# Optimization experiments

Measured on AMD Instinct MI355X. Metric: run time of the kernel, lower is better.

## Reference

```python
import jax, jax.numpy as jnp
import numpy as np

B, IN, H = 65536, 256, 512

def setup_inputs() -> dict:
    key = jax.random.key(0)
    ks = jax.random.split(key, 10)
    inp = {
        "x": jax.random.normal(ks[0], (B, IN), dtype=jnp.float32),
        "h_prev": jax.random.normal(ks[1], (B, H), dtype=jnp.float32),
        "c_prev": jax.random.normal(ks[2], (B, H), dtype=jnp.float32),
        "n_prev": jax.random.uniform(ks[3], (B, H), dtype=jnp.float32),
        "m_prev": jax.random.normal(ks[4], (B, H), dtype=jnp.float32),
        "w_f": jax.random.normal(ks[5], (IN, H), dtype=jnp.float32) * 0.05,
        "w_c": jax.random.normal(ks[6], (IN, H), dtype=jnp.float32) * 0.05,
        "r_f": jax.random.normal(ks[7], (H, H), dtype=jnp.float32) * 0.05,
        "r_c": jax.random.normal(ks[8], (H, H), dtype=jnp.float32) * 0.05,
        "b_f": jnp.zeros((H,), dtype=jnp.float32),
        "b_c": jnp.zeros((H,), dtype=jnp.float32),
    }
    return inp

def reference(x, h_prev, c_prev, n_prev, m_prev, w_f, w_c, r_f, r_c, b_f, b_c):
    # f_t = exp(pre_f); log(f_t) = pre_f, so stabilizer works on pre-activations.
    pre_f = x @ w_f + h_prev @ r_f + b_f          # [B, H]
    c_tilda = x @ w_c + h_prev @ r_c + b_c        # [B, H]
    # m_t = max(log f_t + m_prev, log(exp(0))) = max(pre_f + m_prev, 0)
    m_t = jnp.maximum(pre_f + m_prev, 0.0)
    i_prime = jnp.exp(-m_t)
    f_prime = jnp.exp(pre_f + m_prev - m_t)
    c_t = f_prime * c_prev + i_prime * jnp.tanh(c_tilda)
    n_t = f_prime * n_prev + i_prime
    h_t = jnp.tanh(c_t / jnp.maximum(n_t, 1e-8))
    return (h_t, c_t, n_t, m_t)
```

## Files before the change

kernel.cpp:

```cpp
#include <hip/hip_runtime.h>

#define B_SZ   65536
#define IN_SZ  256
#define H_SZ   512
#define K_SZ   768
#define BM     128
#define BN     128
#define BK     64
#define LDK    72

typedef __attribute__((ext_vector_type(4))) float  f32x4;
typedef __attribute__((ext_vector_type(8))) __bf16 bf16x8;

__device__ __forceinline__ unsigned short f2bf(float f) {
    unsigned u = __float_as_uint(f);
    u += 0x7FFFu + ((u >> 16) & 1u);
    return (unsigned short)(u >> 16);
}

__device__ __forceinline__ float tanh_fast(float x) {
    x = fminf(fmaxf(x, -16.0f), 16.0f);
    float e = __expf(2.0f * x);
    return (e - 1.0f) / (e + 1.0f);
}

__global__ void prep_weights(const float* __restrict__ w_f, const float* __restrict__ w_c,
                             const float* __restrict__ r_f, const float* __restrict__ r_c,
                             unsigned short* __restrict__ wt) {
    int id = blockIdx.x * 256 + threadIdx.x;
    int n  = id / K_SZ;
    int k  = id - n * K_SZ;
    int col = n & (H_SZ - 1);
    float v;
    if (n < H_SZ) v = (k < IN_SZ) ? w_f[k * H_SZ + col] : r_f[(k - IN_SZ) * H_SZ + col];
    else          v = (k < IN_SZ) ? w_c[k * H_SZ + col] : r_c[(k - IN_SZ) * H_SZ + col];
    wt[(size_t)n * K_SZ + k] = f2bf(v);
}

__launch_bounds__(256, 2)
__global__ void smgu_kernel(const float* __restrict__ x, const float* __restrict__ h_prev,
                            const float* __restrict__ c_prev, const float* __restrict__ n_prev,
                            const float* __restrict__ m_prev,
                            const float* __restrict__ b_f, const float* __restrict__ b_c,
                            const unsigned short* __restrict__ wt,
                            float* __restrict__ out) {
    __shared__ unsigned short sA[BM * LDK];
    __shared__ unsigned short sF[BN * LDK];
    __shared__ unsigned short sC[BN * LDK];

    const int tid    = threadIdx.x;
    const int bid    = blockIdx.x;
    const int tile_m = bid >> 2;
    const int tile_n = bid & 3;
    const int m0 = tile_m * BM;
    const int n0 = tile_n * BN;

    const int lane = tid & 63;
    const int wave = tid >> 6;
    const int wm = (wave >> 1) * 64;
    const int wn = (wave & 1) * 64;

    const int fr = lane & 15;
    const int fg = (lane >> 4) * 8;

    f32x4 accF[4][4];
    f32x4 accC[4][4];
#pragma unroll
    for (int i = 0; i < 4; ++i)
#pragma unroll
        for (int j = 0; j < 4; ++j) { accF[i][j] = (f32x4)0.0f; accC[i][j] = (f32x4)0.0f; }

    for (int kb = 0; kb < K_SZ; kb += BK) {
        {
            const float* src; int ldsrc, kloc;
            if (kb < IN_SZ) { src = x;      ldsrc = IN_SZ; kloc = kb; }
            else            { src = h_prev; ldsrc = H_SZ;  kloc = kb - IN_SZ; }
#pragma unroll
            for (int j = 0; j < 8; ++j) {
                int idx = tid + 256 * j;
                int row = idx >> 4, c4 = idx & 15;
                const float4 v = *(const float4*)&src[(size_t)(m0 + row) * ldsrc + kloc + c4 * 4];
                ushort4 b;
                b.x = f2bf(v.x); b.y = f2bf(v.y); b.z = f2bf(v.z); b.w = f2bf(v.w);
                *(ushort4*)&sA[row * LDK + c4 * 4] = b;
            }
        }
#pragma unroll
        for (int j = 0; j < 4; ++j) {
            int idx = tid + 256 * j;
            int row = idx >> 3, c8 = idx & 7;
            uint4 vf = *(const uint4*)&wt[(size_t)(n0 + row) * K_SZ + kb + c8 * 8];
            *(uint4*)&sF[row * LDK + c8 * 8] = vf;
            uint4 vc = *(const uint4*)&wt[(size_t)(H_SZ + n0 + row) * K_SZ + kb + c8 * 8];
            *(uint4*)&sC[row * LDK + c8 * 8] = vc;
        }
        __syncthreads();

#pragma unroll
        for (int ks = 0; ks < BK; ks += 32) {
            bf16x8 af[4], bf[4], bc[4];
#pragma unroll
            for (int mi = 0; mi < 4; ++mi)
                af[mi] = *(const bf16x8*)&sA[(wm + mi * 16 + fr) * LDK + ks + fg];
#pragma unroll
            for (int ni = 0; ni < 4; ++ni) {
                bf[ni] = *(const bf16x8*)&sF[(wn + ni * 16 + fr) * LDK + ks + fg];
                bc[ni] = *(const bf16x8*)&sC[(wn + ni * 16 + fr) * LDK + ks + fg];
            }
#pragma unroll
            for (int mi = 0; mi < 4; ++mi)
#pragma unroll
                for (int ni = 0; ni < 4; ++ni) {
                    accF[mi][ni] = __builtin_amdgcn_mfma_f32_16x16x32_bf16(af[mi], bf[ni], accF[mi][ni], 0, 0, 0);
                    accC[mi][ni] = __builtin_amdgcn_mfma_f32_16x16x32_bf16(af[mi], bc[ni], accC[mi][ni], 0, 0, 0);
                }
        }
        __syncthreads();
    }

    const size_t BH = (size_t)B_SZ * H_SZ;
#pragma unroll
    for (int ni = 0; ni < 4; ++ni) {
        int col = n0 + wn + ni * 16 + fr;
        float bfv = b_f[col], bcv = b_c[col];
#pragma unroll
        for (int mi = 0; mi < 4; ++mi) {
            int row0 = m0 + wm + mi * 16 + (lane >> 4) * 4;
#pragma unroll
            for (int r = 0; r < 4; ++r) {
                size_t idx = (size_t)(row0 + r) * H_SZ + col;
                float pre_f = accF[mi][ni][r] + bfv;
                float pre_c = accC[mi][ni][r] + bcv;
                float mp = m_prev[idx];
                float s  = pre_f + mp;
                float m_t = fmaxf(s, 0.0f);
                float ip  = __expf(-m_t);
                float fp  = __expf(s - m_t);
                float cp  = c_prev[idx];
                float np  = n_prev[idx];
                float c_t = fp * cp + ip * tanh_fast(pre_c);
                float n_t = fp * np + ip;
                float h_t = tanh_fast(c_t / fmaxf(n_t, 1e-8f));
                out[idx]          = h_t;
                out[BH + idx]     = c_t;
                out[2 * BH + idx] = n_t;
                out[3 * BH + idx] = m_t;
            }
        }
    }
}

extern "C" void kernel_launch(void* const* d_in, const int* in_sizes, int n_in,
                              void* d_out, int out_size, void* d_ws, size_t ws_size,
                              hipStream_t stream) {
    const float* x      = (const float*)d_in[0];
    const float* h_prev = (const float*)d_in[1];
    const float* c_prev = (const float*)d_in[2];
    const float* n_prev = (const float*)d_in[3];
    const float* m_prev = (const float*)d_in[4];
    const float* w_f    = (const float*)d_in[5];
    const float* w_c    = (const float*)d_in[6];
    const float* r_f    = (const float*)d_in[7];
    const float* r_c    = (const float*)d_in[8];
    const float* b_f    = (const float*)d_in[9];
    const float* b_c    = (const float*)d_in[10];
    float* out = (float*)d_out;
    unsigned short* wt = (unsigned short*)d_ws;

    prep_weights<<<(2 * H_SZ * K_SZ) / 256, 256, 0, stream>>>(w_f, w_c, r_f, r_c, wt);
    smgu_kernel<<<(B_SZ / BM) * (H_SZ / BN), 256, 0, stream>>>(
        x, h_prev, c_prev, n_prev, m_prev, b_f, b_c, wt, out);
}
```

Baseline: 1.295 ms.

## Restructure SMGU GEMM to full-width N tiles with direct-global weights and LDS-staged epilogue

```diff
diff --git a/kernel.cpp b/kernel.cpp
--- a/kernel.cpp
+++ b/kernel.cpp
@@ -4,13 +4,14 @@
 #define IN_SZ  256
 #define H_SZ   512
 #define K_SZ   768
-#define BM     128
-#define BN     128
+#define BM     64
 #define BK     64
 #define LDK    72
+#define NCHUNK (K_SZ / BK)
 
-typedef __attribute__((ext_vector_type(4))) float  f32x4;
-typedef __attribute__((ext_vector_type(8))) __bf16 bf16x8;
+typedef __attribute__((ext_vector_type(4))) float          f32x4;
+typedef __attribute__((ext_vector_type(8))) __bf16         bf16x8;
+typedef __attribute__((ext_vector_type(4))) unsigned short u16x4;
 
 __device__ __forceinline__ unsigned short f2bf(float f) {
     unsigned u = __float_as_uint(f);
@@ -37,115 +38,129 @@
     wt[(size_t)n * K_SZ + k] = f2bf(v);
 }
 
-__launch_bounds__(256, 2)
+__launch_bounds__(512, 2)
 __global__ void smgu_kernel(const float* __restrict__ x, const float* __restrict__ h_prev,
                             const float* __restrict__ c_prev, const float* __restrict__ n_prev,
                             const float* __restrict__ m_prev,
                             const float* __restrict__ b_f, const float* __restrict__ b_c,
                             const unsigned short* __restrict__ wt,
                             float* __restrict__ out) {
-    __shared__ unsigned short sA[BM * LDK];
-    __shared__ unsigned short sF[BN * LDK];
-    __shared__ unsigned short sC[BN * LDK];
+    __shared__ __align__(16) unsigned char smem[65536];
+    unsigned short* sA = (unsigned short*)smem;
+    float*          eW = (float*)smem;
 
-    const int tid    = threadIdx.x;
-    const int bid    = blockIdx.x;
-    const int tile_m = bid >> 2;
-    const int tile_n = bid & 3;
-    const int m0 = tile_m * BM;
-    const int n0 = tile_n * BN;
-
+    const int tid  = threadIdx.x;
+    const int m0   = blockIdx.x * BM;
     const int lane = tid & 63;
     const int wave = tid >> 6;
-    const int wm = (wave >> 1) * 64;
-    const int wn = (wave & 1) * 64;
+    const int n0   = wave * 64;
+    const int fr   = lane & 15;
+    const int fg   = (lane >> 4) * 8;
+    const int g    = lane >> 4;
 
-    const int fr = lane & 15;
-    const int fg = (lane >> 4) * 8;
-
-    f32x4 accF[4][4];
-    f32x4 accC[4][4];
+    f32x4 accF[4][4], accC[4][4];
 #pragma unroll
     for (int i = 0; i < 4; ++i)
 #pragma unroll
         for (int j = 0; j < 4; ++j) { accF[i][j] = (f32x4)0.0f; accC[i][j] = (f32x4)0.0f; }
 
-    for (int kb = 0; kb < K_SZ; kb += BK) {
-        {
-            const float* src; int ldsrc, kloc;
-            if (kb < IN_SZ) { src = x;      ldsrc = IN_SZ; kloc = kb; }
-            else            { src = h_prev; ldsrc = H_SZ;  kloc = kb - IN_SZ; }
-#pragma unroll
-            for (int j = 0; j < 8; ++j) {
-                int idx = tid + 256 * j;
-                int row = idx >> 4, c4 = idx & 15;
-                const float4 v = *(const float4*)&src[(size_t)(m0 + row) * ldsrc + kloc + c4 * 4];
-                ushort4 b;
-                b.x = f2bf(v.x); b.y = f2bf(v.y); b.z = f2bf(v.z); b.w = f2bf(v.w);
-                *(ushort4*)&sA[row * LDK + c4 * 4] = b;
-            }
-        }
-#pragma unroll
-        for (int j = 0; j < 4; ++j) {
-            int idx = tid + 256 * j;
-            int row = idx >> 3, c8 = idx & 7;
-            uint4 vf = *(const uint4*)&wt[(size_t)(n0 + row) * K_SZ + kb + c8 * 8];
-            *(uint4*)&sF[row * LDK + c8 * 8] = vf;
-            uint4 vc = *(const uint4*)&wt[(size_t)(H_SZ + n0 + row) * K_SZ + kb + c8 * 8];
-            *(uint4*)&sC[row * LDK + c8 * 8] = vc;
-        }
-        __syncthreads();
+    const int r0s = tid >> 4;
+    const int c4s = tid & 15;
 
+    f32x4 pv0, pv1;
+    auto load_chunk = [&](int kb) {
+        const float* src; int ld, kl;
+        if (kb < IN_SZ) { src = x;      ld = IN_SZ; kl = kb; }
+        else            { src = h_prev; ld = H_SZ;  kl = kb - IN_SZ; }
+        pv0 = __builtin_nontemporal_load(
+            (const f32x4*)&src[(size_t)(m0 + r0s) * ld + kl + c4s * 4]);
+        pv1 = __builtin_nontemporal_load(
+            (const f32x4*)&src[(size_t)(m0 + 32 + r0s) * ld + kl + c4s * 4]);
+    };
+    auto write_chunk = [&](int buf) {
+        u16x4 w0, w1;
+        w0[0] = f2bf(pv0[0]); w0[1] = f2bf(pv0[1]); w0[2] = f2bf(pv0[2]); w0[3] = f2bf(pv0[3]);
+        w1[0] = f2bf(pv1[0]); w1[1] = f2bf(pv1[1]); w1[2] = f2bf(pv1[2]); w1[3] = f2bf(pv1[3]);
+        *(u16x4*)&sA[(buf * BM + r0s) * LDK + c4s * 4]      = w0;
+        *(u16x4*)&sA[(buf * BM + 32 + r0s) * LDK + c4s * 4] = w1;
+    };
+
+    load_chunk(0);
+    write_chunk(0);
+    __syncthreads();
+
+    for (int t = 0; t < NCHUNK; ++t) {
+        const int cur = t & 1;
+        if (t + 1 < NCHUNK) load_chunk((t + 1) * BK);
+        const unsigned short* sAc = &sA[cur * BM * LDK];
 #pragma unroll
         for (int ks = 0; ks < BK; ks += 32) {
-            bf16x8 af[4], bf[4], bc[4];
+            bf16x8 af[4], bfx[4], bcx[4];
 #pragma unroll
             for (int mi = 0; mi < 4; ++mi)
-                af[mi] = *(const bf16x8*)&sA[(wm + mi * 16 + fr) * LDK + ks + fg];
+                af[mi] = *(const bf16x8*)&sAc[(mi * 16 + fr) * LDK + ks + fg];
+            const int kk = t * BK + ks + fg;
 #pragma unroll
             for (int ni = 0; ni < 4; ++ni) {
-                bf[ni] = *(const bf16x8*)&sF[(wn + ni * 16 + fr) * LDK + ks + fg];
-                bc[ni] = *(const bf16x8*)&sC[(wn + ni * 16 + fr) * LDK + ks + fg];
+                const int nr = n0 + ni * 16 + fr;
+                bfx[ni] = *(const bf16x8*)&wt[(size_t)nr * K_SZ + kk];
+                bcx[ni] = *(const bf16x8*)&wt[(size_t)(H_SZ + nr) * K_SZ + kk];
             }
 #pragma unroll
             for (int mi = 0; mi < 4; ++mi)
 #pragma unroll
                 for (int ni = 0; ni < 4; ++ni) {
-                    accF[mi][ni] = __builtin_amdgcn_mfma_f32_16x16x32_bf16(af[mi], bf[ni], accF[mi][ni], 0, 0, 0);
-                    accC[mi][ni] = __builtin_amdgcn_mfma_f32_16x16x32_bf16(af[mi], bc[ni], accC[mi][ni], 0, 0, 0);
+                    accF[mi][ni] = __builtin_amdgcn_mfma_f32_16x16x32_bf16(af[mi], bfx[ni], accF[mi][ni], 0, 0, 0);
+                    accC[mi][ni] = __builtin_amdgcn_mfma_f32_16x16x32_bf16(af[mi], bcx[ni], accC[mi][ni], 0, 0, 0);
                 }
         }
+        if (t + 1 < NCHUNK) write_chunk(cur ^ 1);
         __syncthreads();
     }
 
+    float* ef = eW + wave * 2048;
+    float* ec = ef + 1024;
+    const f32x4 bfv = *(const f32x4*)&b_f[n0 + fr * 4];
+    const f32x4 bcv = *(const f32x4*)&b_c[n0 + fr * 4];
     const size_t BH = (size_t)B_SZ * H_SZ;
+
+#pragma unroll 1
+    for (int mi = 0; mi < 4; ++mi) {
 #pragma unroll
-    for (int ni = 0; ni < 4; ++ni) {
-        int col = n0 + wn + ni * 16 + fr;
-        float bfv = b_f[col], bcv = b_c[col];
-#pragma unroll
-        for (int mi = 0; mi < 4; ++mi) {
-            int row0 = m0 + wm + mi * 16 + (lane >> 4) * 4;
+        for (int ni = 0; ni < 4; ++ni)
 #pragma unroll
             for (int r = 0; r < 4; ++r) {
-                size_t idx = (size_t)(row0 + r) * H_SZ + col;
-                float pre_f = accF[mi][ni][r] + bfv;
-                float pre_c = accC[mi][ni][r] + bcv;
-                float mp = m_prev[idx];
-                float s  = pre_f + mp;
-                float m_t = fmaxf(s, 0.0f);
-                float ip  = __expf(-m_t);
-                float fp  = __expf(s - m_t);
-                float cp  = c_prev[idx];
-                float np  = n_prev[idx];
-                float c_t = fp * cp + ip * tanh_fast(pre_c);
-                float n_t = fp * np + ip;
-                float h_t = tanh_fast(c_t / fmaxf(n_t, 1e-8f));
-                out[idx]          = h_t;
-                out[BH + idx]     = c_t;
-                out[2 * BH + idx] = n_t;
-                out[3 * BH + idx] = m_t;
+                const int ri = g * 4 + r;
+                const int cc = ni * 16 + fr;
+                ef[ri * 64 + cc] = accF[mi][ni][r];
+                ec[ri * 64 + cc] = accC[mi][ni][r];
             }
+#pragma unroll
+        for (int rr = 0; rr < 4; ++rr) {
+            const int ri = rr * 4 + g;
+            const size_t idx = (size_t)(m0 + mi * 16 + ri) * H_SZ + n0 + fr * 4;
+            f32x4 pF = *(const f32x4*)&ef[ri * 64 + fr * 4];
+            f32x4 pC = *(const f32x4*)&ec[ri * 64 + fr * 4];
+            f32x4 cp = __builtin_nontemporal_load((const f32x4*)&c_prev[idx]);
+            f32x4 np = __builtin_nontemporal_load((const f32x4*)&n_prev[idx]);
+            f32x4 mp = __builtin_nontemporal_load((const f32x4*)&m_prev[idx]);
+            f32x4 ho, co, no, mo;
+#pragma unroll
+            for (int q = 0; q < 4; ++q) {
+                float preF = pF[q] + bfv[q];
+                float s    = preF + mp[q];
+                float mt   = fmaxf(s, 0.0f);
+                float ipv  = __expf(-mt);
+                float fpv  = __expf(s - mt);
+                float ct   = fpv * cp[q] + ipv * tanh_fast(pC[q] + bcv[q]);
+                float ntv  = fpv * np[q] + ipv;
+                float htv  = tanh_fast(ct / fmaxf(ntv, 1e-8f));
+                ho[q] = htv; co[q] = ct; no[q] = ntv; mo[q] = mt;
+            }
+            __builtin_nontemporal_store(ho, (f32x4*)&out[idx]);
+            __builtin_nontemporal_store(co, (f32x4*)&out[BH + idx]);
+            __builtin_nontemporal_store(no, (f32x4*)&out[2 * BH + idx]);
+            __builtin_nontemporal_store(mo, (f32x4*)&out[3 * BH + idx]);
         }
     }
 }
@@ -168,6 +183,6 @@
     unsigned short* wt = (unsigned short*)d_ws;
 
     prep_weights<<<(2 * H_SZ * K_SZ) / 256, 256, 0, stream>>>(w_f, w_c, r_f, r_c, wt);
-    smgu_kernel<<<(B_SZ / BM) * (H_SZ / BN), 256, 0, stream>>>(
+    smgu_kernel<<<B_SZ / BM, 512, 0, stream>>>(
         x, h_prev, c_prev, n_prev, m_prev, b_f, b_c, wt, out);
 }
```

Result: slower. 1.665 ms (+28.6%).
